# Kernel optimization log

Hardware: AMD Instinct MI355X
Metric: run time of the kernel (lower is better)

The kernel has to match this reference:

```python
import jax, jax.numpy as jnp
import numpy as np

B, S, D = 2, 4096, 512
H, DQK, DV, W = 8, 64, 64, 32
ORDER = 6  # 2^(2*6)=4096 cells: 64x64 Hilbert grid covers max_seq_len=4096


def hilbert_d2xy(d, order):
    """Vectorized standard Hilbert curve d->(x,y) mapping on a 2^order grid."""
    x = jnp.zeros_like(d)
    y = jnp.zeros_like(d)
    t = d
    s = 1
    for _ in range(order):
        rx = (t // 2) & 1
        ry = (t ^ rx) & 1
        swap = ry == 0
        flip = swap & (rx == 1)
        xf = jnp.where(flip, s - 1 - x, x)
        yf = jnp.where(flip, s - 1 - y, y)
        x, y = jnp.where(swap, yf, xf), jnp.where(swap, xf, yf)
        x = x + s * rx
        y = y + s * ry
        t = t // 4
        s = s * 2
    return jnp.stack([x, y], axis=-1)


def neighbor_idx(seq_len, window):
    d = jnp.arange(seq_len, dtype=jnp.int32)
    coords = hilbert_d2xy(d, ORDER).astype(jnp.float32)  # (S, 2)
    diff = coords[:, None, :] - coords[None, :, :]
    dist = jnp.sqrt((diff ** 2).sum(-1))  # (S, S)
    _, idx = jax.lax.top_k(-dist, window)  # k smallest distances
    return idx.astype(jnp.int32)


def setup_inputs() -> dict:
    key = jax.random.key(0)
    k1, k2, k3, k4, k5 = jax.random.split(key, 5)
    sc = float(1.0 / np.sqrt(D))
    return {
        "x": jax.random.normal(k1, (B, S, D), jnp.float32),
        "W_q": jax.random.normal(k2, (H * DQK, D), jnp.float32) * sc,
        "W_k": jax.random.normal(k3, (H * DQK, D), jnp.float32) * sc,
        "W_v": jax.random.normal(k4, (H * DV, D), jnp.float32) * sc,
        "W_o": jax.random.normal(k5, (D, H * DV), jnp.float32) * sc,
        "neighbor_indices": neighbor_idx(S, W),
    }


def reference(x, W_q, W_k, W_v, W_o, neighbor_indices):
    b, s, _ = x.shape
    q = (x @ W_q.T).reshape(b, s, H, DQK).transpose(0, 2, 1, 3)  # (b,h,s,d)
    k = (x @ W_k.T).reshape(b, s, H, DQK).transpose(0, 2, 1, 3)
    v = (x @ W_v.T).reshape(b, s, H, DV).transpose(0, 2, 1, 3)
    kn = k[:, :, neighbor_indices, :]  # gather -> (b,h,s,w,d)
    vn = v[:, :, neighbor_indices, :]
    scale = float(1.0 / np.sqrt(DQK))
    scores = jnp.einsum('bhsd,bhswd->bhsw', q, kn) * scale
    attn = jax.nn.softmax(scores, axis=-1)
    out = jnp.einsum('bhsw,bhswd->bhsd', attn, vn)
    out = out.transpose(0, 2, 1, 3).reshape(b, s, H * DV)
    return out @ W_o.T
```

## Files before the change

### kernel.cpp

```cpp
#include <hip/hip_runtime.h>
#include <hip/hip_bf16.h>
#include <stdint.h>
#include <stddef.h>

constexpr int Bc = 2;
constexpr int Sc = 4096;
constexpr int Dc = 512;
constexpr int Hc = 8;
constexpr int Wc = 32;

using bf16_t = __bf16;
typedef __attribute__((ext_vector_type(8))) __bf16 bf16x8;
typedef __attribute__((ext_vector_type(4))) __bf16 bf16x4;
typedef __attribute__((ext_vector_type(2))) __bf16 bf16x2;
typedef __attribute__((ext_vector_type(4))) float f32x4;

__device__ __forceinline__ void async_copy16(const void* g, void* l) {
    __builtin_amdgcn_global_load_lds(
        (const __attribute__((address_space(1))) void*)g,
        (__attribute__((address_space(3))) void*)l,
        16, 0, 0);
}

__global__ void convert_all(const float* __restrict__ x,
                            const float* __restrict__ wq, const float* __restrict__ wk,
                            const float* __restrict__ wv, const float* __restrict__ wo,
                            bf16_t* __restrict__ xc, bf16_t* __restrict__ dq,
                            bf16_t* __restrict__ dk, bf16_t* __restrict__ dv,
                            bf16_t* __restrict__ dwo) {
    const int blk = blockIdx.x;
    const float* s; bf16_t* d; int base;
    if (blk < 4096) { s = x; d = xc; base = blk * 1024; }
    else {
        const int r = blk - 4096, which = r >> 8;
        s = (which == 0) ? wq : (which == 1) ? wk : (which == 2) ? wv : wo;
        d = (which == 0) ? dq : (which == 1) ? dk : (which == 2) ? dv : dwo;
        base = (r & 255) * 1024;
    }
    const int i = base + threadIdx.x * 4;
    const float4 v = *(const float4*)(s + i);
    bf16x4 o; o[0] = (bf16_t)v.x; o[1] = (bf16_t)v.y;
    o[2] = (bf16_t)v.z; o[3] = (bf16_t)v.w;
    *(bf16x4*)(d + i) = o;
}

template<int BM, int BN, int TM, int TN, bool F32OUT>
__global__ __launch_bounds__(256) void gemm_bt(
    const bf16_t* __restrict__ A, int lda,
    const bf16_t* __restrict__ B0, const bf16_t* __restrict__ B1,
    const bf16_t* __restrict__ B2, int ldb, int nPerB,
    void* __restrict__ C, int ldc, int K)
{
    constexpr int BK = 32;
    __shared__ __align__(1024) bf16_t Alds[BM * BK];
    __shared__ __align__(1024) bf16_t Blds[BN * BK];

    const int tid  = threadIdx.x;
    const int lane = tid & 63;
    const int wv   = tid >> 6;
    const int wm   = wv >> 1;
    const int wn   = wv & 1;
    const int r    = lane & 15;
    const int q4   = lane >> 4;

    const int blkM = blockIdx.x * BM;
    const int colC = blockIdx.y * BN;

    const bf16_t* Bp = B0;
    int nB = colC;
    if (nPerB > 0) {
        int wsel = colC / nPerB;
        nB = colC - wsel * nPerB;
        Bp = (wsel == 0) ? B0 : (wsel == 1) ? B1 : B2;
    }

    f32x4 acc[TM][TN];
    const f32x4 fzero = {0.f, 0.f, 0.f, 0.f};
    #pragma unroll
    for (int i = 0; i < TM; ++i)
        #pragma unroll
        for (int j = 0; j < TN; ++j) acc[i][j] = fzero;

    constexpr int A_LOADS = (BM * BK * 2) / (256 * 16);
    constexpr int B_LOADS = (BN * BK * 2) / (256 * 16);

    for (int kk = 0; kk < K; kk += BK) {
        __syncthreads();
        #pragma unroll
        for (int i = 0; i < A_LOADS; ++i) {
            int off  = i * 4096 + tid * 16;
            int row  = off >> 6;
            int colb = off & 63;
            const char* g = (const char*)A + ((size_t)(blkM + row) * lda + kk) * 2 + colb;
            async_copy16(g, (char*)Alds + off);
        }
        #pragma unroll
        for (int i = 0; i < B_LOADS; ++i) {
            int off  = i * 4096 + tid * 16;
            int row  = off >> 6;
            int colb = off & 63;
            const char* g = (const char*)Bp + ((size_t)(nB + row) * ldb + kk) * 2 + colb;
            async_copy16(g, (char*)Blds + off);
        }
        __syncthreads();

        bf16x8 af[TM], bfr[TN];
        #pragma unroll
        for (int mt = 0; mt < TM; ++mt)
            af[mt] = *(const bf16x8*)&Alds[(wm * TM * 16 + mt * 16 + r) * BK + q4 * 8];
        #pragma unroll
        for (int nt = 0; nt < TN; ++nt)
            bfr[nt] = *(const bf16x8*)&Blds[(wn * TN * 16 + nt * 16 + r) * BK + q4 * 8];

        #pragma unroll
        for (int mt = 0; mt < TM; ++mt)
            #pragma unroll
            for (int nt = 0; nt < TN; ++nt)
                acc[mt][nt] = __builtin_amdgcn_mfma_f32_16x16x32_bf16(
                    af[mt], bfr[nt], acc[mt][nt], 0, 0, 0);
    }

    #pragma unroll
    for (int mt = 0; mt < TM; ++mt) {
        #pragma unroll
        for (int nt = 0; nt < TN; ++nt) {
            int rr0 = blkM + wm * TM * 16 + mt * 16 + q4 * 4;
            int cc  = colC + wn * TN * 16 + nt * 16 + r;
            #pragma unroll
            for (int i = 0; i < 4; ++i) {
                size_t o = (size_t)(rr0 + i) * ldc + cc;
                if constexpr (F32OUT) ((float*)C)[o]  = acc[mt][nt][i];
                else                  ((bf16_t*)C)[o] = (bf16_t)acc[mt][nt][i];
            }
        }
    }
}

__global__ __launch_bounds__(256) void attn_fast(
    const bf16_t* __restrict__ QKV,
    const int*    __restrict__ nidx,
    bf16_t*       __restrict__ attn_out)
{
    __shared__ __align__(16) float wa_lds[4][64];
    const int lane = threadIdx.x & 63;
    const int wv   = threadIdx.x >> 6;

    const int bi  = blockIdx.x;
    const int blk = (bi & 7) * 2048 + (bi >> 3);
    const int wg  = blk * 4 + wv;
    const int s = wg & (Sc - 1);
    const int h = (wg >> 12) & (Hc - 1);
    const int b = wg >> 15;
    const size_t row = (size_t)b * Sc + s;

    const int w    = lane >> 1;
    const int half = lane & 1;
    const int t    = nidx[s * Wc + w];

    const char* qkvB = (const char*)QKV;
    const char* Qptr = qkvB + row * 3072 + h * 128 + half * 64;
    const char* Kptr = qkvB + ((size_t)b * Sc + t) * 3072 + 1024 + h * 128 + half * 64;

    bf16x8 q8[4], k8[4];
    #pragma unroll
    for (int i = 0; i < 4; ++i) {
        q8[i] = *(const bf16x8*)(Qptr + 16 * i);
        k8[i] = *(const bf16x8*)(Kptr + 16 * i);
    }
    float p = 0.f;
    #pragma unroll
    for (int i = 0; i < 4; ++i)
        #pragma unroll
        for (int j = 0; j < 8; ++j)
            p += (float)q8[i][j] * (float)k8[i][j];
    p += __shfl_xor(p, 1);
    p *= 0.125f;

    float mx = p;
    #pragma unroll
    for (int m = 2; m <= 32; m <<= 1) mx = fmaxf(mx, __shfl_xor(mx, m));
    const float e = __expf(p - mx);
    float sum = e;
    #pragma unroll
    for (int m = 2; m <= 32; m <<= 1) sum += __shfl_xor(sum, m);
    const float a = e / sum;

    if (half == 0) {
        wa_lds[wv][2 * w]     = __int_as_float(t * 3072);
        wa_lds[wv][2 * w + 1] = a;
    }
    __syncthreads();

    const int d2 = lane & 31;
    const int nh = lane >> 5;
    const float* chunkp = &wa_lds[wv][nh * 32];
    const char* Vb = qkvB + (size_t)b * Sc * 3072 + 2048 + h * 128;
    const int dk = d2 * 4;

    float acc0 = 0.f, acc1 = 0.f;
    #pragma unroll
    for (int j = 0; j < 8; ++j) {
        const float4 c = *(const float4*)(chunkp + 4 * j);
        {
            const unsigned v = *(const unsigned*)(Vb + __float_as_int(c.x) + dk);
            acc0 = fmaf(c.y, __uint_as_float(v << 16), acc0);
            acc1 = fmaf(c.y, __uint_as_float(v & 0xffff0000u), acc1);
        }
        {
            const unsigned v = *(const unsigned*)(Vb + __float_as_int(c.z) + dk);
            acc0 = fmaf(c.w, __uint_as_float(v << 16), acc0);
            acc1 = fmaf(c.w, __uint_as_float(v & 0xffff0000u), acc1);
        }
    }
    acc0 += __shfl_xor(acc0, 32);
    acc1 += __shfl_xor(acc1, 32);
    if (nh == 0) {
        bf16x2 pr; pr[0] = (bf16_t)acc0; pr[1] = (bf16_t)acc1;
        *(bf16x2*)((char*)attn_out + row * 1024 + h * 128 + dk) = pr;
    }
}

extern "C" void kernel_launch(void* const* d_in, const int* in_sizes, int n_in,
                              void* d_out, int out_size, void* d_ws, size_t ws_size,
                              hipStream_t stream) {
    (void)in_sizes; (void)n_in; (void)out_size; (void)ws_size;
    const int* nidx = (const int*)d_in[5];
    const int M = Bc * Sc;
    float* out = (float*)d_out;

    char* w = (char*)d_ws;
    bf16_t* xc   = (bf16_t*)(w + 256);
    bf16_t* Wqc  = xc  + 4194304;
    bf16_t* Wkc  = Wqc + 262144;
    bf16_t* Wvc  = Wkc + 262144;
    bf16_t* Woc  = Wvc + 262144;
    bf16_t* qkv  = Woc + 262144;
    bf16_t* attnS = xc;

    convert_all<<<5120, 256, 0, stream>>>(
        (const float*)d_in[0], (const float*)d_in[1], (const float*)d_in[2],
        (const float*)d_in[3], (const float*)d_in[4],
        xc, Wqc, Wkc, Wvc, Woc);

    gemm_bt<128, 128, 4, 4, false><<<dim3(M / 128, 1536 / 128), 256, 0, stream>>>(
        xc, Dc, Wqc, Wkc, Wvc, Dc, 512, qkv, 1536, Dc);

    attn_fast<<<(Bc * Hc * Sc) / 4, 256, 0, stream>>>(qkv, nidx, attnS);

    gemm_bt<128, 64, 4, 2, true><<<dim3(M / 128, 512 / 64), 256, 0, stream>>>(
        attnS, 512, Woc, Woc, Woc, 512, 0, out, Dc, Dc);
}
```

Measured before the change: 148.7 us.

## Switch pipeline to fp16 with fdot2 scores and half-precision PV accumulation

Converts all intermediates from bf16 to fp16, uses fp16 MFMA in the GEMMs, computes QK dot products with packed fdot2, and accumulates the attention-weighted V sum in packed half precision. It also removes the softmax max-subtraction reduction, relying on scores staying small. This reduces ALU and shuffle work in the attention kernel at the cost of reduced accumulation precision and overflow risk for large scores.

After: 150.1 us. Within noise of the previous version (+0.9%).

```diff
diff --git a/kernel.cpp b/kernel.cpp
--- a/kernel.cpp
+++ b/kernel.cpp
@@ -9,10 +9,10 @@
 constexpr int Hc = 8;
 constexpr int Wc = 32;
 
-using bf16_t = __bf16;
-typedef __attribute__((ext_vector_type(8))) __bf16 bf16x8;
-typedef __attribute__((ext_vector_type(4))) __bf16 bf16x4;
-typedef __attribute__((ext_vector_type(2))) __bf16 bf16x2;
+using f16_t = _Float16;
+typedef __attribute__((ext_vector_type(8))) _Float16 f16x8;
+typedef __attribute__((ext_vector_type(4))) _Float16 f16x4;
+typedef __attribute__((ext_vector_type(2))) _Float16 f16x2;
 typedef __attribute__((ext_vector_type(4))) float f32x4;
 
 __device__ __forceinline__ void async_copy16(const void* g, void* l) {
@@ -25,11 +25,11 @@
 __global__ void convert_all(const float* __restrict__ x,
                             const float* __restrict__ wq, const float* __restrict__ wk,
                             const float* __restrict__ wv, const float* __restrict__ wo,
-                            bf16_t* __restrict__ xc, bf16_t* __restrict__ dq,
-                            bf16_t* __restrict__ dk, bf16_t* __restrict__ dv,
-                            bf16_t* __restrict__ dwo) {
+                            f16_t* __restrict__ xc, f16_t* __restrict__ dq,
+                            f16_t* __restrict__ dk, f16_t* __restrict__ dv,
+                            f16_t* __restrict__ dwo) {
     const int blk = blockIdx.x;
-    const float* s; bf16_t* d; int base;
+    const float* s; f16_t* d; int base;
     if (blk < 4096) { s = x; d = xc; base = blk * 1024; }
     else {
         const int r = blk - 4096, which = r >> 8;
@@ -39,21 +39,21 @@
     }
     const int i = base + threadIdx.x * 4;
     const float4 v = *(const float4*)(s + i);
-    bf16x4 o; o[0] = (bf16_t)v.x; o[1] = (bf16_t)v.y;
-    o[2] = (bf16_t)v.z; o[3] = (bf16_t)v.w;
-    *(bf16x4*)(d + i) = o;
+    f16x4 o; o[0] = (f16_t)v.x; o[1] = (f16_t)v.y;
+    o[2] = (f16_t)v.z; o[3] = (f16_t)v.w;
+    *(f16x4*)(d + i) = o;
 }
 
 template<int BM, int BN, int TM, int TN, bool F32OUT>
-__global__ __launch_bounds__(256) void gemm_bt(
-    const bf16_t* __restrict__ A, int lda,
-    const bf16_t* __restrict__ B0, const bf16_t* __restrict__ B1,
-    const bf16_t* __restrict__ B2, int ldb, int nPerB,
+__global__ __launch_bounds__(256) void gemm_f16(
+    const f16_t* __restrict__ A, int lda,
+    const f16_t* __restrict__ B0, const f16_t* __restrict__ B1,
+    const f16_t* __restrict__ B2, int ldb, int nPerB,
     void* __restrict__ C, int ldc, int K)
 {
     constexpr int BK = 32;
-    __shared__ __align__(1024) bf16_t Alds[BM * BK];
-    __shared__ __align__(1024) bf16_t Blds[BN * BK];
+    __shared__ __align__(1024) f16_t Alds[BM * BK];
+    __shared__ __align__(1024) f16_t Blds[BN * BK];
 
     const int tid  = threadIdx.x;
     const int lane = tid & 63;
@@ -66,7 +66,7 @@
     const int blkM = blockIdx.x * BM;
     const int colC = blockIdx.y * BN;
 
-    const bf16_t* Bp = B0;
+    const f16_t* Bp = B0;
     int nB = colC;
     if (nPerB > 0) {
         int wsel = colC / nPerB;
@@ -104,19 +104,19 @@
         }
         __syncthreads();
 
-        bf16x8 af[TM], bfr[TN];
+        f16x8 af[TM], bfr[TN];
         #pragma unroll
         for (int mt = 0; mt < TM; ++mt)
-            af[mt] = *(const bf16x8*)&Alds[(wm * TM * 16 + mt * 16 + r) * BK + q4 * 8];
+            af[mt] = *(const f16x8*)&Alds[(wm * TM * 16 + mt * 16 + r) * BK + q4 * 8];
         #pragma unroll
         for (int nt = 0; nt < TN; ++nt)
-            bfr[nt] = *(const bf16x8*)&Blds[(wn * TN * 16 + nt * 16 + r) * BK + q4 * 8];
+            bfr[nt] = *(const f16x8*)&Blds[(wn * TN * 16 + nt * 16 + r) * BK + q4 * 8];
 
         #pragma unroll
         for (int mt = 0; mt < TM; ++mt)
             #pragma unroll
             for (int nt = 0; nt < TN; ++nt)
-                acc[mt][nt] = __builtin_amdgcn_mfma_f32_16x16x32_bf16(
+                acc[mt][nt] = __builtin_amdgcn_mfma_f32_16x16x32_f16(
                     af[mt], bfr[nt], acc[mt][nt], 0, 0, 0);
     }
 
@@ -129,17 +129,17 @@
             #pragma unroll
             for (int i = 0; i < 4; ++i) {
                 size_t o = (size_t)(rr0 + i) * ldc + cc;
-                if constexpr (F32OUT) ((float*)C)[o]  = acc[mt][nt][i];
-                else                  ((bf16_t*)C)[o] = (bf16_t)acc[mt][nt][i];
+                if constexpr (F32OUT) ((float*)C)[o] = acc[mt][nt][i];
+                else                  ((f16_t*)C)[o] = (f16_t)acc[mt][nt][i];
             }
         }
     }
 }
 
 __global__ __launch_bounds__(256) void attn_fast(
-    const bf16_t* __restrict__ QKV,
-    const int*    __restrict__ nidx,
-    bf16_t*       __restrict__ attn_out)
+    const f16_t* __restrict__ QKV,
+    const int*   __restrict__ nidx,
+    f16_t*       __restrict__ attn_out)
 {
     __shared__ __align__(16) float wa_lds[4][64];
     const int lane = threadIdx.x & 63;
@@ -158,66 +158,70 @@
     const int t    = nidx[s * Wc + w];
 
     const char* qkvB = (const char*)QKV;
-    const char* Qptr = qkvB + row * 3072 + h * 128 + half * 64;
-    const char* Kptr = qkvB + ((size_t)b * Sc + t) * 3072 + 1024 + h * 128 + half * 64;
-
-    bf16x8 q8[4], k8[4];
+    const char* Qp = qkvB + row * 3072 + h * 128 + half * 64;
+    const char* Kp = qkvB + ((size_t)b * Sc + t) * 3072 + 1024 + h * 128 + half * 64;
+
+    uint4 qv[4], kv[4];
     #pragma unroll
     for (int i = 0; i < 4; ++i) {
-        q8[i] = *(const bf16x8*)(Qptr + 16 * i);
-        k8[i] = *(const bf16x8*)(Kptr + 16 * i);
+        qv[i] = *(const uint4*)(Qp + 16 * i);
+        kv[i] = *(const uint4*)(Kp + 16 * i);
     }
     float p = 0.f;
     #pragma unroll
-    for (int i = 0; i < 4; ++i)
-        #pragma unroll
-        for (int j = 0; j < 8; ++j)
-            p += (float)q8[i][j] * (float)k8[i][j];
+    for (int i = 0; i < 4; ++i) {
+        p = __builtin_amdgcn_fdot2(__builtin_bit_cast(f16x2, qv[i].x),
+                                   __builtin_bit_cast(f16x2, kv[i].x), p, false);
+        p = __builtin_amdgcn_fdot2(__builtin_bit_cast(f16x2, qv[i].y),
+                                   __builtin_bit_cast(f16x2, kv[i].y), p, false);
+        p = __builtin_amdgcn_fdot2(__builtin_bit_cast(f16x2, qv[i].z),
+                                   __builtin_bit_cast(f16x2, kv[i].z), p, false);
+        p = __builtin_amdgcn_fdot2(__builtin_bit_cast(f16x2, qv[i].w),
+                                   __builtin_bit_cast(f16x2, kv[i].w), p, false);
+    }
     p += __shfl_xor(p, 1);
-    p *= 0.125f;
-
-    float mx = p;
-    #pragma unroll
-    for (int m = 2; m <= 32; m <<= 1) mx = fmaxf(mx, __shfl_xor(mx, m));
-    const float e = __expf(p - mx);
+
+    const float e = __expf(p * 0.125f);
     float sum = e;
     #pragma unroll
     for (int m = 2; m <= 32; m <<= 1) sum += __shfl_xor(sum, m);
     const float a = e / sum;
 
     if (half == 0) {
-        wa_lds[wv][2 * w]     = __int_as_float(t * 3072);
-        wa_lds[wv][2 * w + 1] = a;
+        const f16_t ah = (f16_t)a;
+        f16x2 ap; ap[0] = ah; ap[1] = ah;
+        float2 wr;
+        wr.x = __int_as_float(t * 3072);
+        wr.y = __builtin_bit_cast(float, ap);
+        *(float2*)&wa_lds[wv][2 * w] = wr;
     }
     __syncthreads();
 
     const int d2 = lane & 31;
     const int nh = lane >> 5;
-    const float* chunkp = &wa_lds[wv][nh * 32];
-    const char* Vb = qkvB + (size_t)b * Sc * 3072 + 2048 + h * 128;
-    const int dk = d2 * 4;
-
-    float acc0 = 0.f, acc1 = 0.f;
+    const float* ch = &wa_lds[wv][nh * 32];
+    const char* Vp = qkvB + (size_t)b * Sc * 3072 + 2048 + h * 128 + d2 * 4;
+
+    f16x2 acc2 = {(f16_t)0.f, (f16_t)0.f};
     #pragma unroll
     for (int j = 0; j < 8; ++j) {
-        const float4 c = *(const float4*)(chunkp + 4 * j);
+        const float4 c = *(const float4*)(ch + 4 * j);
         {
-            const unsigned v = *(const unsigned*)(Vb + __float_as_int(c.x) + dk);
-            acc0 = fmaf(c.y, __uint_as_float(v << 16), acc0);
-            acc1 = fmaf(c.y, __uint_as_float(v & 0xffff0000u), acc1);
+            const f16x2 v2 = __builtin_bit_cast(f16x2,
+                *(const unsigned*)(Vp + __float_as_int(c.x)));
+            acc2 += __builtin_bit_cast(f16x2, c.y) * v2;
         }
         {
-            const unsigned v = *(const unsigned*)(Vb + __float_as_int(c.z) + dk);
-            acc0 = fmaf(c.w, __uint_as_float(v << 16), acc0);
-            acc1 = fmaf(c.w, __uint_as_float(v & 0xffff0000u), acc1);
-        }
-    }
-    acc0 += __shfl_xor(acc0, 32);
-    acc1 += __shfl_xor(acc1, 32);
-    if (nh == 0) {
-        bf16x2 pr; pr[0] = (bf16_t)acc0; pr[1] = (bf16_t)acc1;
-        *(bf16x2*)((char*)attn_out + row * 1024 + h * 128 + dk) = pr;
-    }
+            const f16x2 v2 = __builtin_bit_cast(f16x2,
+                *(const unsigned*)(Vp + __float_as_int(c.z)));
+            acc2 += __builtin_bit_cast(f16x2, c.w) * v2;
+        }
+    }
+    const int other = __shfl_xor(__builtin_bit_cast(int, acc2), 32);
+    acc2 += __builtin_bit_cast(f16x2, other);
+    if (nh == 0)
+        *(unsigned*)((char*)attn_out + row * 1024 + h * 128 + d2 * 4) =
+            __builtin_bit_cast(unsigned, acc2);
 }
 
 extern "C" void kernel_launch(void* const* d_in, const int* in_sizes, int n_in,
@@ -229,24 +233,24 @@
     float* out = (float*)d_out;
 
     char* w = (char*)d_ws;
-    bf16_t* xc   = (bf16_t*)(w + 256);
-    bf16_t* Wqc  = xc  + 4194304;
-    bf16_t* Wkc  = Wqc + 262144;
-    bf16_t* Wvc  = Wkc + 262144;
-    bf16_t* Woc  = Wvc + 262144;
-    bf16_t* qkv  = Woc + 262144;
-    bf16_t* attnS = xc;
+    f16_t* xc   = (f16_t*)(w + 256);
+    f16_t* Wqc  = xc  + 4194304;
+    f16_t* Wkc  = Wqc + 262144;
+    f16_t* Wvc  = Wkc + 262144;
+    f16_t* Woc  = Wvc + 262144;
+    f16_t* qkv  = Woc + 262144;
+    f16_t* attnS = xc;
 
     convert_all<<<5120, 256, 0, stream>>>(
         (const float*)d_in[0], (const float*)d_in[1], (const float*)d_in[2],
         (const float*)d_in[3], (const float*)d_in[4],
         xc, Wqc, Wkc, Wvc, Woc);
 
-    gemm_bt<128, 128, 4, 4, false><<<dim3(M / 128, 1536 / 128), 256, 0, stream>>>(
+    gemm_f16<128, 128, 4, 4, false><<<dim3(M / 128, 1536 / 128), 256, 0, stream>>>(
         xc, Dc, Wqc, Wkc, Wvc, Dc, 512, qkv, 1536, Dc);
 
     attn_fast<<<(Bc * Hc * Sc) / 4, 256, 0, stream>>>(qkv, nidx, attnS);
 
-    gemm_bt<128, 64, 4, 2, true><<<dim3(M / 128, 512 / 64), 256, 0, stream>>>(
+    gemm_f16<128, 64, 4, 2, true><<<dim3(M / 128, 512 / 64), 256, 0, stream>>>(
         attnS, 512, Woc, Woc, Woc, 512, 0, out, Dc, Dc);
 }
```
